# Kernel tuning notes

Hardware: AMD Instinct MI355X
Metric: run time of the kernel (lower is better)

## Reference

```python
import jax, jax.numpy as jnp
import numpy as np

N_NODES = 100000
IN_C = 512
OUT_C = 128
ITERATIONS = 3
NNZ_FEAT = 2_000_000
N_EDGES = 1_600_000


def setup_inputs() -> dict:
    key = jax.random.key(0)
    k1, k2, k3, k4, k5, k6, k7 = jax.random.split(key, 7)
    # sparse feature matrix: COO indices [2, nnz] (row in [0,N_NODES), col in [0,IN_C))
    f_rows = jax.random.randint(k1, (NNZ_FEAT,), 0, N_NODES)
    f_cols = jax.random.randint(k2, (NNZ_FEAT,), 0, IN_C)
    # force the max indices to be present so feature_count == (N_NODES, IN_C)
    f_rows = f_rows.at[-1].set(N_NODES - 1)
    f_cols = f_cols.at[-1].set(IN_C - 1)
    feat_indices = jnp.stack([f_rows, f_cols]).astype(jnp.int64)
    feat_values = jax.random.uniform(k3, (NNZ_FEAT,), dtype=jnp.float32)
    # sparse normalized adjacency: COO indices [2, n_edges]
    a_rows = jax.random.randint(k4, (N_EDGES,), 0, N_NODES)
    a_cols = jax.random.randint(k5, (N_EDGES,), 0, N_NODES)
    adj_indices = jnp.stack([a_rows, a_cols]).astype(jnp.int64)
    # normalized weights ~ 1/degree scale
    adj_values = jax.random.uniform(k6, (N_EDGES,), dtype=jnp.float32) / 16.0
    # learned parameters (xavier-uniform style scale)
    wb = float(np.sqrt(6.0 / (IN_C + OUT_C)))
    weight = jax.random.uniform(k7, (IN_C, OUT_C), minval=-wb, maxval=wb, dtype=jnp.float32)
    bias = jax.random.uniform(jax.random.fold_in(key, 99), (1, OUT_C), minval=-wb, maxval=wb, dtype=jnp.float32)
    return {
        "feat_indices": feat_indices,
        "feat_values": feat_values,
        "adj_indices": adj_indices,
        "adj_values": adj_values,
        "weight": weight,
        "bias": bias,
    }


def reference(feat_indices, feat_values, adj_indices, adj_values, weight, bias):
    # spmm(feat_indices, feat_values, N, IN_C, weight): sparse [N, IN_C] @ dense [IN_C, OUT_C]
    f_rows, f_cols = feat_indices[0], feat_indices[1]
    msgs = feat_values[:, None] * weight[f_cols]              # [nnz, OUT_C]
    base = jax.ops.segment_sum(msgs, f_rows, num_segments=N_NODES)  # [N, OUT_C]
    base = base + bias
    # dropout in eval mode (training=False) is identity
    base = jax.nn.relu(base)
    a_rows, a_cols = adj_indices[0], adj_indices[1]
    for _ in range(ITERATIONS - 1):
        # sparse [N, N] @ dense [N, OUT_C]
        base = jax.ops.segment_sum(adj_values[:, None] * base[a_cols], a_rows, num_segments=N_NODES)
    return base
```

## Files before the change

kernel.cpp:

```cpp
#include <hip/hip_runtime.h>

#define N_NODES 100000
#define VROWS   200000
#define BSHIFT  8
#define BROWS   256
#define NBUCK   ((VROWS + BROWS - 1) / BROWS)
#define BINB    256
#define NBAND   8
#define SBINS   (BROWS * NBAND)

static __device__ __forceinline__ unsigned short f2bf(float x) {
    unsigned u = __float_as_uint(x);
    return (unsigned short)((u + 0x7fffu + ((u >> 16) & 1u)) >> 16);
}
static __device__ __forceinline__ float bf_lo(unsigned u) { return __uint_as_float(u << 16); }
static __device__ __forceinline__ float bf_hi(unsigned u) { return __uint_as_float(u & 0xffff0000u); }

static __device__ __forceinline__ void nt_colval(const long long* p, int& c, float& v) {
    long long e = __builtin_nontemporal_load(p);
    c = (int)(e & 0x1ffffLL);
    v = __uint_as_float((unsigned)((unsigned long long)e >> 32));
}

static __device__ __forceinline__ long long pack_cv(int col, int rl, float v) {
    unsigned lo = (unsigned)col | ((unsigned)rl << 17);
    return (long long)lo | ((long long)(unsigned)__float_as_uint(v) << 32);
}


__global__ void zero_small_kernel(int* __restrict__ p, int n) {
    int i = blockIdx.x * blockDim.x + threadIdx.x;
    if (i < n) p[i] = 0;
}

__global__ __launch_bounds__(256) void binA_kernel(
        const int* __restrict__ f_rows, const int* __restrict__ a_rows,
        int* __restrict__ cur, int* __restrict__ pbb, int nnzf, int nedge) {
    __shared__ int hist[NBUCK];
    const int t = threadIdx.x;
    for (int b = t; b < NBUCK; b += 256) hist[b] = 0;
    __syncthreads();
    {
        const int per = (nnzf + BINB - 1) / BINB;
        const int beg = blockIdx.x * per;
        const int end = min(beg + per, nnzf);
        int i = beg + t;
        for (; i + 3 * 256 < end; i += 4 * 256) {
            int r0 = f_rows[i], r1 = f_rows[i + 256], r2 = f_rows[i + 512], r3 = f_rows[i + 768];
            atomicAdd(&hist[r0 >> BSHIFT], 1);
            atomicAdd(&hist[r1 >> BSHIFT], 1);
            atomicAdd(&hist[r2 >> BSHIFT], 1);
            atomicAdd(&hist[r3 >> BSHIFT], 1);
        }
        for (; i < end; i += 256) atomicAdd(&hist[f_rows[i] >> BSHIFT], 1);
    }
    {
        const int per = (nedge + BINB - 1) / BINB;
        const int beg = blockIdx.x * per;
        const int end = min(beg + per, nedge);
        int i = beg + t;
        for (; i + 3 * 256 < end; i += 4 * 256) {
            int r0 = a_rows[i] + N_NODES, r1 = a_rows[i + 256] + N_NODES;
            int r2 = a_rows[i + 512] + N_NODES, r3 = a_rows[i + 768] + N_NODES;
            atomicAdd(&hist[r0 >> BSHIFT], 1);
            atomicAdd(&hist[r1 >> BSHIFT], 1);
            atomicAdd(&hist[r2 >> BSHIFT], 1);
            atomicAdd(&hist[r3 >> BSHIFT], 1);
        }
        for (; i < end; i += 256) atomicAdd(&hist[(a_rows[i] + N_NODES) >> BSHIFT], 1);
    }
    __syncthreads();
    for (int b = t; b < NBUCK; b += 256) {
        int c = hist[b];
        pbb[blockIdx.x * NBUCK + b] = c ? atomicAdd(&cur[b], c) : 0;
    }
}

__global__ void bucket_scan_kernel(const int* __restrict__ cur, int* __restrict__ bbase,
                                   int* __restrict__ rp) {
    __shared__ int sh[1024];
    const int t = threadIdx.x;
    int v = (t < NBUCK) ? cur[t] : 0;
    sh[t] = v;
    __syncthreads();
    for (int off = 1; off < 1024; off <<= 1) {
        int u = (t >= off) ? sh[t - off] : 0;
        __syncthreads();
        sh[t] += u;
        __syncthreads();
    }
    if (t < NBUCK) bbase[t] = sh[t] - v;
    if (t == NBUCK - 1) rp[VROWS] = sh[t];
}

__global__ __launch_bounds__(256) void binB_kernel(
        const int* __restrict__ f_rows, const int* __restrict__ f_cols, const float* __restrict__ f_vals,
        const int* __restrict__ a_rows, const int* __restrict__ a_cols, const float* __restrict__ a_vals,
        const int* __restrict__ bbase, const int* __restrict__ pbb,
        long long* __restrict__ staging, int nnzf, int nedge) {
    __shared__ int curs[NBUCK];
    const int t = threadIdx.x;
    for (int b = t; b < NBUCK; b += 256) curs[b] = bbase[b] + pbb[blockIdx.x * NBUCK + b];
    __syncthreads();
    {
        const int per = (nnzf + BINB - 1) / BINB;
        const int beg = blockIdx.x * per;
        const int end = min(beg + per, nnzf);
        for (int i = beg + t; i < end; i += 256) {
            const int   r = f_rows[i];
            const int   c = f_cols[i];
            const float v = f_vals[i];
            const int p = atomicAdd(&curs[r >> BSHIFT], 1);
            staging[p] = pack_cv(c, r & (BROWS - 1), v);
        }
    }
    {
        const int per = (nedge + BINB - 1) / BINB;
        const int beg = blockIdx.x * per;
        const int end = min(beg + per, nedge);
        for (int i = beg + t; i < end; i += 256) {
            const int   r = a_rows[i] + N_NODES;
            const int   c = a_cols[i];
            const float v = a_vals[i];
            const int p = atomicAdd(&curs[r >> BSHIFT], 1);
            staging[p] = pack_cv(c, r & (BROWS - 1), v);
        }
    }
}

__global__ __launch_bounds__(256) void sort_kernel(
        const int* __restrict__ cur, const int* __restrict__ bbase,
        const long long* __restrict__ staging, long long* __restrict__ colval,
        int* __restrict__ rp) {
    const int b = blockIdx.x;
    const int t = threadIdx.x;
    __shared__ int cnt[SBINS];
    __shared__ int tsum[256];
    const int n = cur[b];
    const int base = bbase[b];
    for (int k = t; k < SBINS; k += 256) cnt[k] = 0;
    __syncthreads();
    const long long* seg = staging + base;
    for (int j = t; j < n; j += 256) {
        unsigned lo = (unsigned)(seg[j] & 0xffffffffLL);
        const int rl = (lo >> 17) & (BROWS - 1);
        const int band = (int)((lo & 0x1ffffu) >> 14);
        atomicAdd(&cnt[rl * NBAND + band], 1);
    }
    __syncthreads();
    int loc[NBAND];
    int s = 0;
    #pragma unroll
    for (int k = 0; k < NBAND; ++k) { loc[k] = s; s += cnt[t * NBAND + k]; }
    tsum[t] = s;
    __syncthreads();
    for (int o = 1; o < 256; o <<= 1) {
        int u = (t >= o) ? tsum[t - o] : 0;
        __syncthreads();
        tsum[t] += u;
        __syncthreads();
    }
    const int texcl = (t == 0) ? 0 : tsum[t - 1];
    const int row = (b << BSHIFT) + t;
    if (row < VROWS) rp[row] = base + texcl;
    #pragma unroll
    for (int k = 0; k < NBAND; ++k) cnt[t * NBAND + k] = base + texcl + loc[k];
    __syncthreads();
    for (int j = t; j < n; j += 256) {
        long long e = seg[j];
        unsigned lo = (unsigned)(e & 0xffffffffLL);
        const int rl = (lo >> 17) & (BROWS - 1);
        const int band = (int)((lo & 0x1ffffu) >> 14);
        const int p = atomicAdd(&cnt[rl * NBAND + band], 1);
        colval[p] = (long long)(lo & 0x1ffffu) | (e & 0xffffffff00000000LL);
    }
}


__global__ __launch_bounds__(256) void spmm_feat_kernel(
        const int* __restrict__ row_ptr, const long long* __restrict__ colval,
        const float* __restrict__ W, const float* __restrict__ bias,
        unsigned short* __restrict__ base_bf, int n) {
    const int wave = (blockIdx.x * blockDim.x + threadIdx.x) >> 6;
    const int lane = threadIdx.x & 63;
    const int h = lane >> 5;
    const int s = lane & 31;
    const int r = wave * 2 + h;
    const float4* __restrict__ W4 = (const float4*)W;
    float4 a0 = make_float4(0.f, 0.f, 0.f, 0.f), a1 = a0;
    int i = 0, end = 0;
    if (r < n) { i = row_ptr[r]; end = row_ptr[r + 1]; }
    for (; i + 1 < end; i += 2) {
        int c0, c1; float v0, v1;
        nt_colval(colval + i,     c0, v0);
        nt_colval(colval + i + 1, c1, v1);
        const float4 w0 = W4[c0 * 32 + s];
        const float4 w1 = W4[c1 * 32 + s];
        a0.x += v0 * w0.x; a0.y += v0 * w0.y; a0.z += v0 * w0.z; a0.w += v0 * w0.w;
        a1.x += v1 * w1.x; a1.y += v1 * w1.y; a1.z += v1 * w1.z; a1.w += v1 * w1.w;
    }
    if (i < end) {
        int c; float v;
        nt_colval(colval + i, c, v);
        const float4 w = W4[c * 32 + s];
        a0.x += v * w.x; a0.y += v * w.y; a0.z += v * w.z; a0.w += v * w.w;
    }
    if (r < n) {
        const float4 b = ((const float4*)bias)[s];
        ushort4 o;
        o.x = f2bf(fmaxf(a0.x + a1.x + b.x, 0.f));
        o.y = f2bf(fmaxf(a0.y + a1.y + b.y, 0.f));
        o.z = f2bf(fmaxf(a0.z + a1.z + b.z, 0.f));
        o.w = f2bf(fmaxf(a0.w + a1.w + b.w, 0.f));
        ((ushort4*)(base_bf + (size_t)r * 128))[s] = o;
    }
}


__global__ __launch_bounds__(256) void spmm_adj_bf_bf_kernel(
        const int* __restrict__ row_ptr, const long long* __restrict__ colval,
        const uint2* __restrict__ src, unsigned short* __restrict__ dst, int n) {
    const int wave = (blockIdx.x * blockDim.x + threadIdx.x) >> 6;
    const int lane = threadIdx.x & 63;
    const int h = lane >> 5;
    const int s = lane & 31;
    const int r = wave * 2 + h;
    float4 a0 = make_float4(0.f, 0.f, 0.f, 0.f), a1 = a0;
    int i = 0, end = 0;
    if (r < n) { i = row_ptr[r]; end = row_ptr[r + 1]; }
    for (; i + 1 < end; i += 2) {
        int c0, c1; float v0, v1;
        nt_colval(colval + i,     c0, v0);
        nt_colval(colval + i + 1, c1, v1);
        const uint2 u0 = src[c0 * 32 + s];
        const uint2 u1 = src[c1 * 32 + s];
        a0.x += v0 * bf_lo(u0.x); a0.y += v0 * bf_hi(u0.x);
        a0.z += v0 * bf_lo(u0.y); a0.w += v0 * bf_hi(u0.y);
        a1.x += v1 * bf_lo(u1.x); a1.y += v1 * bf_hi(u1.x);
        a1.z += v1 * bf_lo(u1.y); a1.w += v1 * bf_hi(u1.y);
    }
    if (i < end) {
        int c; float v;
        nt_colval(colval + i, c, v);
        const uint2 u = src[c * 32 + s];
        a0.x += v * bf_lo(u.x); a0.y += v * bf_hi(u.x);
        a0.z += v * bf_lo(u.y); a0.w += v * bf_hi(u.y);
    }
    if (r < n) {
        ushort4 o;
        o.x = f2bf(a0.x + a1.x); o.y = f2bf(a0.y + a1.y);
        o.z = f2bf(a0.z + a1.z); o.w = f2bf(a0.w + a1.w);
        ((ushort4*)(dst + (size_t)r * 128))[s] = o;
    }
}


__global__ __launch_bounds__(256) void spmm_adj_bf_f32_kernel(
        const int* __restrict__ row_ptr, const long long* __restrict__ colval,
        const uint2* __restrict__ src, float* __restrict__ dst, int n) {
    const int wave = (blockIdx.x * blockDim.x + threadIdx.x) >> 6;
    const int lane = threadIdx.x & 63;
    const int h = lane >> 5;
    const int s = lane & 31;
    const int r = wave * 2 + h;
    float4 a0 = make_float4(0.f, 0.f, 0.f, 0.f), a1 = a0;
    int i = 0, end = 0;
    if (r < n) { i = row_ptr[r]; end = row_ptr[r + 1]; }
    for (; i + 1 < end; i += 2) {
        int c0, c1; float v0, v1;
        nt_colval(colval + i,     c0, v0);
        nt_colval(colval + i + 1, c1, v1);
        const uint2 u0 = src[c0 * 32 + s];
        const uint2 u1 = src[c1 * 32 + s];
        a0.x += v0 * bf_lo(u0.x); a0.y += v0 * bf_hi(u0.x);
        a0.z += v0 * bf_lo(u0.y); a0.w += v0 * bf_hi(u0.y);
        a1.x += v1 * bf_lo(u1.x); a1.y += v1 * bf_hi(u1.x);
        a1.z += v1 * bf_lo(u1.y); a1.w += v1 * bf_hi(u1.y);
    }
    if (i < end) {
        int c; float v;
        nt_colval(colval + i, c, v);
        const uint2 u = src[c * 32 + s];
        a0.x += v * bf_lo(u.x); a0.y += v * bf_hi(u.x);
        a0.z += v * bf_lo(u.y); a0.w += v * bf_hi(u.y);
    }
    if (r < n) {
        float4 acc;
        acc.x = a0.x + a1.x; acc.y = a0.y + a1.y;
        acc.z = a0.z + a1.z; acc.w = a0.w + a1.w;
        ((float4*)(dst + (size_t)r * 128))[s] = acc;
    }
}


extern "C" void kernel_launch(void* const* d_in, const int* in_sizes, int n_in,
                              void* d_out, int out_size, void* d_ws, size_t ws_size,
                              hipStream_t stream) {
    const int*   fi   = (const int*)d_in[0];
    const float* fv   = (const float*)d_in[1];
    const int*   ai   = (const int*)d_in[2];
    const float* av   = (const float*)d_in[3];
    const float* W    = (const float*)d_in[4];
    const float* bias = (const float*)d_in[5];
    float* out = (float*)d_out;

    const int nnzf  = in_sizes[1];
    const int nedge = in_sizes[3];
    const int ntot  = nnzf + nedge;
    const int* f_rows = fi;
    const int* f_cols = fi + nnzf;
    const int* a_rows = ai;
    const int* a_cols = ai + nedge;

    char* wp = (char*)d_ws;
    auto balloc = [&](size_t bytes) -> char* {
        char* p = wp;
        wp += (bytes + 255) & ~(size_t)255;
        return p;
    };
    long long* staging = (long long*)balloc(8ull * (size_t)ntot);
    unsigned short* base_bf = (unsigned short*)staging;
    unsigned short* t1 = (unsigned short*)balloc(2ull * N_NODES * 128);
    long long* colval = (long long*)balloc(8ull * (size_t)ntot);
    int* rp    = (int*)balloc(4ull * (VROWS + 1));
    int* cur   = (int*)balloc(4ull * NBUCK);
    int* bbase = (int*)balloc(4ull * NBUCK);
    int* pbb   = (int*)balloc(4ull * BINB * NBUCK);

    const int nwaves = (N_NODES + 1) / 2;
    const int RW = (nwaves + 3) / 4;

    zero_small_kernel<<<(NBUCK + 255) / 256, 256, 0, stream>>>(cur, NBUCK);
    binA_kernel<<<BINB, 256, 0, stream>>>(f_rows, a_rows, cur, pbb, nnzf, nedge);
    bucket_scan_kernel<<<1, 1024, 0, stream>>>(cur, bbase, rp);
    binB_kernel<<<BINB, 256, 0, stream>>>(f_rows, f_cols, fv, a_rows, a_cols, av,
                                          bbase, pbb, staging, nnzf, nedge);
    sort_kernel<<<NBUCK, 256, 0, stream>>>(cur, bbase, staging, colval, rp);

    spmm_feat_kernel<<<RW, 256, 0, stream>>>(rp, colval, W, bias, base_bf, N_NODES);
    spmm_adj_bf_bf_kernel<<<RW, 256, 0, stream>>>(rp + N_NODES, colval,
                                                  (const uint2*)base_bf, t1, N_NODES);
    spmm_adj_bf_f32_kernel<<<RW, 256, 0, stream>>>(rp + N_NODES, colval,
                                                   (const uint2*)t1, out, N_NODES);
}
```

Baseline: 338.5 us.

## Stage weight matrix in LDS as bf16 halves for feature SpMM

The sort kernel now bands feature entries by column half (col>>8) and records a per-row split point, so each row's nonzeros are grouped into columns 0-255 and 256-511. A new feature SpMM kernel with 1024-thread blocks loads each half of W into shared memory as bf16 (64KB), then processes 128 rows per block against it. This replaces global/L2 gathers of fp32 W rows with LDS reads. The cost is W being reloaded and converted by every block, extra barriers, and reduced precision of W in the first layer.

```diff
diff --git a/kernel.cpp b/kernel.cpp
--- a/kernel.cpp
+++ b/kernel.cpp
@@ -8,6 +8,7 @@
 #define BINB    256
 #define NBAND   8
 #define SBINS   (BROWS * NBAND)
+#define FRPB    128
 
 static __device__ __forceinline__ unsigned short f2bf(float x) {
     unsigned u = __float_as_uint(x);
@@ -131,7 +132,7 @@
 __global__ __launch_bounds__(256) void sort_kernel(
         const int* __restrict__ cur, const int* __restrict__ bbase,
         const long long* __restrict__ staging, long long* __restrict__ colval,
-        int* __restrict__ rp) {
+        int* __restrict__ rp, int* __restrict__ fsplit) {
     const int b = blockIdx.x;
     const int t = threadIdx.x;
     __shared__ int cnt[SBINS];
@@ -144,7 +145,9 @@
     for (int j = t; j < n; j += 256) {
         unsigned lo = (unsigned)(seg[j] & 0xffffffffLL);
         const int rl = (lo >> 17) & (BROWS - 1);
-        const int band = (int)((lo & 0x1ffffu) >> 14);
+        const int col = (int)(lo & 0x1ffffu);
+        const int vrow = (b << BSHIFT) + rl;
+        const int band = (vrow < N_NODES) ? (col >> 8) : (col >> 14);
         atomicAdd(&cnt[rl * NBAND + band], 1);
     }
     __syncthreads();
@@ -163,6 +166,7 @@
     const int texcl = (t == 0) ? 0 : tsum[t - 1];
     const int row = (b << BSHIFT) + t;
     if (row < VROWS) rp[row] = base + texcl;
+    if (row < N_NODES) fsplit[row] = base + texcl + loc[1];
     #pragma unroll
     for (int k = 0; k < NBAND; ++k) cnt[t * NBAND + k] = base + texcl + loc[k];
     __syncthreads();
@@ -170,48 +174,83 @@
         long long e = seg[j];
         unsigned lo = (unsigned)(e & 0xffffffffLL);
         const int rl = (lo >> 17) & (BROWS - 1);
-        const int band = (int)((lo & 0x1ffffu) >> 14);
+        const int col = (int)(lo & 0x1ffffu);
+        const int vrow = (b << BSHIFT) + rl;
+        const int band = (vrow < N_NODES) ? (col >> 8) : (col >> 14);
         const int p = atomicAdd(&cnt[rl * NBAND + band], 1);
-        colval[p] = (long long)(lo & 0x1ffffu) | (e & 0xffffffff00000000LL);
-    }
-}
-
-
-__global__ __launch_bounds__(256) void spmm_feat_kernel(
-        const int* __restrict__ row_ptr, const long long* __restrict__ colval,
+        colval[p] = (long long)(unsigned)col | (e & 0xffffffff00000000LL);
+    }
+}
+
+
+__global__ __launch_bounds__(1024) void spmm_feat_lds_kernel(
+        const int* __restrict__ rp, const int* __restrict__ fsplit,
+        const long long* __restrict__ colval,
         const float* __restrict__ W, const float* __restrict__ bias,
         unsigned short* __restrict__ base_bf, int n) {
-    const int wave = (blockIdx.x * blockDim.x + threadIdx.x) >> 6;
-    const int lane = threadIdx.x & 63;
+    __shared__ uint2 lds[8192];
+    const int t = threadIdx.x;
+    const int lane = t & 63;
     const int h = lane >> 5;
     const int s = lane & 31;
-    const int r = wave * 2 + h;
-    const float4* __restrict__ W4 = (const float4*)W;
-    float4 a0 = make_float4(0.f, 0.f, 0.f, 0.f), a1 = a0;
-    int i = 0, end = 0;
-    if (r < n) { i = row_ptr[r]; end = row_ptr[r + 1]; }
-    for (; i + 1 < end; i += 2) {
-        int c0, c1; float v0, v1;
-        nt_colval(colval + i,     c0, v0);
-        nt_colval(colval + i + 1, c1, v1);
-        const float4 w0 = W4[c0 * 32 + s];
-        const float4 w1 = W4[c1 * 32 + s];
-        a0.x += v0 * w0.x; a0.y += v0 * w0.y; a0.z += v0 * w0.z; a0.w += v0 * w0.w;
-        a1.x += v1 * w1.x; a1.y += v1 * w1.y; a1.z += v1 * w1.z; a1.w += v1 * w1.w;
-    }
-    if (i < end) {
-        int c; float v;
-        nt_colval(colval + i, c, v);
-        const float4 w = W4[c * 32 + s];
-        a0.x += v * w.x; a0.y += v * w.y; a0.z += v * w.z; a0.w += v * w.w;
-    }
-    if (r < n) {
-        const float4 b = ((const float4*)bias)[s];
+    const int rbase = blockIdx.x * FRPB + (((t >> 6) << 1) + h) * 4;
+    float4 acc[4];
+    #pragma unroll
+    for (int k = 0; k < 4; ++k) acc[k] = make_float4(0.f, 0.f, 0.f, 0.f);
+
+    for (int p = 0; p < 2; ++p) {
+        if (p) __syncthreads();
+        {
+            const float4* Wg = (const float4*)W + p * 8192;
+            #pragma unroll
+            for (int j = 0; j < 8; ++j) {
+                float4 f = Wg[j * 1024 + t];
+                uint2 u;
+                u.x = (unsigned)f2bf(f.x) | ((unsigned)f2bf(f.y) << 16);
+                u.y = (unsigned)f2bf(f.z) | ((unsigned)f2bf(f.w) << 16);
+                lds[j * 1024 + t] = u;
+            }
+        }
+        __syncthreads();
+        #pragma unroll
+        for (int k = 0; k < 4; ++k) {
+            const int r = rbase + k;
+            if (r >= n) break;
+            int i        = p ? fsplit[r] : rp[r];
+            const int end = p ? rp[r + 1] : fsplit[r];
+            float4 a0 = make_float4(0.f, 0.f, 0.f, 0.f), a1 = a0;
+            for (; i + 1 < end; i += 2) {
+                int c0, c1; float v0, v1;
+                nt_colval(colval + i,     c0, v0);
+                nt_colval(colval + i + 1, c1, v1);
+                const uint2 u0 = lds[(c0 & 255) * 32 + s];
+                const uint2 u1 = lds[(c1 & 255) * 32 + s];
+                a0.x += v0 * bf_lo(u0.x); a0.y += v0 * bf_hi(u0.x);
+                a0.z += v0 * bf_lo(u0.y); a0.w += v0 * bf_hi(u0.y);
+                a1.x += v1 * bf_lo(u1.x); a1.y += v1 * bf_hi(u1.x);
+                a1.z += v1 * bf_lo(u1.y); a1.w += v1 * bf_hi(u1.y);
+            }
+            if (i < end) {
+                int c; float v;
+                nt_colval(colval + i, c, v);
+                const uint2 u = lds[(c & 255) * 32 + s];
+                a0.x += v * bf_lo(u.x); a0.y += v * bf_hi(u.x);
+                a0.z += v * bf_lo(u.y); a0.w += v * bf_hi(u.y);
+            }
+            acc[k].x += a0.x + a1.x; acc[k].y += a0.y + a1.y;
+            acc[k].z += a0.z + a1.z; acc[k].w += a0.w + a1.w;
+        }
+    }
+    const float4 b = ((const float4*)bias)[s];
+    #pragma unroll
+    for (int k = 0; k < 4; ++k) {
+        const int r = rbase + k;
+        if (r >= n) break;
         ushort4 o;
-        o.x = f2bf(fmaxf(a0.x + a1.x + b.x, 0.f));
-        o.y = f2bf(fmaxf(a0.y + a1.y + b.y, 0.f));
-        o.z = f2bf(fmaxf(a0.z + a1.z + b.z, 0.f));
-        o.w = f2bf(fmaxf(a0.w + a1.w + b.w, 0.f));
+        o.x = f2bf(fmaxf(acc[k].x + b.x, 0.f));
+        o.y = f2bf(fmaxf(acc[k].y + b.y, 0.f));
+        o.z = f2bf(fmaxf(acc[k].z + b.z, 0.f));
+        o.w = f2bf(fmaxf(acc[k].w + b.w, 0.f));
         ((ushort4*)(base_bf + (size_t)r * 128))[s] = o;
     }
 }
@@ -322,22 +361,25 @@
     unsigned short* base_bf = (unsigned short*)staging;
     unsigned short* t1 = (unsigned short*)balloc(2ull * N_NODES * 128);
     long long* colval = (long long*)balloc(8ull * (size_t)ntot);
-    int* rp    = (int*)balloc(4ull * (VROWS + 1));
-    int* cur   = (int*)balloc(4ull * NBUCK);
-    int* bbase = (int*)balloc(4ull * NBUCK);
-    int* pbb   = (int*)balloc(4ull * BINB * NBUCK);
+    int* rp     = (int*)balloc(4ull * (VROWS + 1));
+    int* fsplit = (int*)balloc(4ull * N_NODES);
+    int* cur    = (int*)balloc(4ull * NBUCK);
+    int* bbase  = (int*)balloc(4ull * NBUCK);
+    int* pbb    = (int*)balloc(4ull * BINB * NBUCK);
 
     const int nwaves = (N_NODES + 1) / 2;
     const int RW = (nwaves + 3) / 4;
+    const int FB = (N_NODES + FRPB - 1) / FRPB;
 
     zero_small_kernel<<<(NBUCK + 255) / 256, 256, 0, stream>>>(cur, NBUCK);
     binA_kernel<<<BINB, 256, 0, stream>>>(f_rows, a_rows, cur, pbb, nnzf, nedge);
     bucket_scan_kernel<<<1, 1024, 0, stream>>>(cur, bbase, rp);
     binB_kernel<<<BINB, 256, 0, stream>>>(f_rows, f_cols, fv, a_rows, a_cols, av,
                                           bbase, pbb, staging, nnzf, nedge);
-    sort_kernel<<<NBUCK, 256, 0, stream>>>(cur, bbase, staging, colval, rp);
-
-    spmm_feat_kernel<<<RW, 256, 0, stream>>>(rp, colval, W, bias, base_bf, N_NODES);
+    sort_kernel<<<NBUCK, 256, 0, stream>>>(cur, bbase, staging, colval, rp, fsplit);
+
+    spmm_feat_lds_kernel<<<FB, 1024, 0, stream>>>(rp, fsplit, colval, W, bias,
+                                                  base_bf, N_NODES);
     spmm_adj_bf_bf_kernel<<<RW, 256, 0, stream>>>(rp + N_NODES, colval,
                                                   (const uint2*)base_bf, t1, N_NODES);
     spmm_adj_bf_f32_kernel<<<RW, 256, 0, stream>>>(rp + N_NODES, colval,
```

After: 342.2 us. No clear change (+1.1%).
